# Kernel tuning notes

Measured on AMD Instinct MI355X. Metric: run time of the kernel, lower is better.

The kernel has to match this reference:

```python
import jax, jax.numpy as jnp
import numpy as np

N = 100000   # nodes
E = 400000   # edges
P = 250000   # permutations (substructures)
L = 16       # lrp_length
D = 16       # lrp_out_dim
M = P * L    # perm-length rows of the sparse gather matrices


def setup_inputs() -> dict:
    key = jax.random.key(0)
    ks = jax.random.split(key, 16)
    return {
        "nfeat": jax.random.normal(ks[0], (N, D), dtype=jnp.float32),
        "efeat_idx": jax.random.randint(ks[1], (E,), 0, 4, dtype=jnp.int64),
        "n_row": jnp.arange(M, dtype=jnp.int64),
        "n_col": jax.random.randint(ks[2], (M,), 0, N, dtype=jnp.int64),
        "n_val": jax.random.uniform(ks[3], (M,), dtype=jnp.float32),
        "e_row": jnp.arange(M, dtype=jnp.int64),
        "e_col": jax.random.randint(ks[4], (M,), 0, E, dtype=jnp.int64),
        "e_val": jax.random.uniform(ks[5], (M,), dtype=jnp.float32),
        "p_row": jax.random.randint(ks[6], (P,), 0, N, dtype=jnp.int64),
        "p_col": jnp.arange(P, dtype=jnp.int64),
        "p_val": jax.random.uniform(ks[7], (P,), dtype=jnp.float32),
        "degs": jax.random.uniform(ks[8], (N,), dtype=jnp.float32) * 10.0,
        "weights": jax.random.normal(ks[9], (D, D, L), dtype=jnp.float32),
        "bias": jnp.zeros((1, D), dtype=jnp.float32),
        "W0": jax.random.normal(ks[10], (1, 2 * D), dtype=jnp.float32),
        "b0": jnp.zeros((2 * D,), dtype=jnp.float32),
        "W1": jax.random.normal(ks[11], (2 * D, D), dtype=jnp.float32),
        "b1": jnp.zeros((D,), dtype=jnp.float32),
        "bond_emb": jax.random.normal(ks[12], (4, D), dtype=jnp.float32),
    }


def _spmm(row, col, val, mat, m):
    # torch_sparse.spmm(index, value, m, n, mat): out[r] += val * mat[c]
    return jax.ops.segment_sum(val[:, None] * mat[col], row, num_segments=m)


def reference(nfeat, efeat_idx, n_row, n_col, n_val, e_row, e_col, e_val,
              p_row, p_col, p_val, degs, weights, bias, W0, b0, W1, b1, bond_emb):
    efeat = bond_emb[efeat_idx]                              # [E, D]
    x = _spmm(n_row, n_col, n_val, nfeat, M) \
        + _spmm(e_row, e_col, e_val, efeat, M)               # [M, D], M = P*L
    # transpose(0,1).view(D, -1, L).permute(1, 2, 0) -> [P, L, D]
    x = x.T.reshape(D, P, L).transpose(1, 2, 0)
    # einsum('dab,bca->dc'): d=P, a=L, b=D_in, c=D_out
    x = jax.nn.relu(jnp.einsum('pld,dcl->pc', x, weights) + bias)  # [P, D]
    pooled = _spmm(p_row, p_col, p_val, x, N)                # [N, D]
    # degree gate MLP: 1 -> 2D -> D
    fd = jax.nn.relu(degs[:, None] @ W0 + b0) @ W1 + b1      # [N, D]
    return pooled * fd
```

## Files before the change

### kernel.cpp

```cpp
#include <hip/hip_runtime.h>

#define NP 250000
#define NN 100000
#define NE 400000
#define LL 16
#define DD 16
#define MM (NP * LL)
#define NTILES (NP / 16)
#define PERM_BLOCKS 512
#define GWAVES (PERM_BLOCKS * 4)

typedef __bf16 bf16x8 __attribute__((ext_vector_type(8)));
typedef float  f32x4  __attribute__((ext_vector_type(4)));
typedef int    i32x4  __attribute__((ext_vector_type(4)));

__device__ __forceinline__ float4 fma4(float a, float4 b, float4 c) {
    float4 r;
    r.x = fmaf(a, b.x, c.x);
    r.y = fmaf(a, b.y, c.y);
    r.z = fmaf(a, b.z, c.z);
    r.w = fmaf(a, b.w, c.w);
    return r;
}

__global__ __launch_bounds__(256) void init_kernel(
    const float* __restrict__ w,
    const float* __restrict__ nfeat,
    const float* __restrict__ bond_emb,
    const int* __restrict__ e_col,
    const int* __restrict__ efeat_idx,
    const float* __restrict__ degs,
    const float* __restrict__ W0,
    const float* __restrict__ b0,
    const float* __restrict__ W1,
    const float* __restrict__ b1,
    __bf16* __restrict__ wfrag,
    __bf16* __restrict__ nfeat_bf,
    __bf16* __restrict__ bond_bf,
    unsigned char* __restrict__ be2,
    float* __restrict__ fd,
    float* __restrict__ out)
{
    int t = blockIdx.x * 256 + threadIdx.x;
    if (t < 4096) {
        int kb = t >> 9;
        int lane = (t >> 3) & 63;
        int j = t & 7;
        int quad = lane >> 4, c = lane & 15;
        int d = ((quad & 1) << 3) + j;
        int l = ((quad >> 1) << 3) + kb;
        wfrag[t] = (__bf16)w[d * 256 + c * 16 + l];
    }
    if (t < NN * DD) {
        nfeat_bf[t] = (__bf16)nfeat[t];
        out[t] = 0.f;
    }
    if (t < 64) bond_bf[t] = (__bf16)bond_emb[t];
    if (t < MM / 4) {
        int4 ec = *(const int4*)(e_col + t * 4);
        unsigned int c0 = (unsigned int)efeat_idx[ec.x] & 3u;
        unsigned int c1 = (unsigned int)efeat_idx[ec.y] & 3u;
        unsigned int c2 = (unsigned int)efeat_idx[ec.z] & 3u;
        unsigned int c3 = (unsigned int)efeat_idx[ec.w] & 3u;
        be2[t] = (unsigned char)(c0 | (c1 << 2) | (c2 << 4) | (c3 << 6));
    }
    if (fd != nullptr && t < NN) {
        float dg = degs[t];
        float4 a0 = ((const float4*)b1)[0];
        float4 a1 = ((const float4*)b1)[1];
        float4 a2 = ((const float4*)b1)[2];
        float4 a3 = ((const float4*)b1)[3];
#pragma unroll
        for (int j2 = 0; j2 < 32; ++j2) {
            float h = fmaxf(fmaf(dg, W0[j2], b0[j2]), 0.f);
            const float4* w1r = (const float4*)(W1 + j2 * 16);
            a0 = fma4(h, w1r[0], a0);
            a1 = fma4(h, w1r[1], a1);
            a2 = fma4(h, w1r[2], a2);
            a3 = fma4(h, w1r[3], a3);
        }
        float4* o = (float4*)(fd + (size_t)t * DD);
        o[0] = a0; o[1] = a1; o[2] = a2; o[3] = a3;
    }
}


struct Early { i32x4 nca, ncb, pr; };
struct Late  { f32x4 nva, nvb, eva, evb, pv; unsigned int be16; };
struct Gath  { bf16x8 nfr[8]; float gv[4]; int prs[4]; };

__device__ __forceinline__ void load_early(Early& e, int tile, int col, int lhalf, int quad,
        const int* __restrict__ n_col, const int* __restrict__ p_row) {
    const int pbase = tile * 16;
    const int mbase = (pbase + col) * LL + lhalf * 8;
    e.nca = __builtin_nontemporal_load((const i32x4*)(n_col + mbase));
    e.ncb = __builtin_nontemporal_load((const i32x4*)(n_col + mbase + 4));
    e.pr  = __builtin_nontemporal_load((const i32x4*)(p_row + pbase + quad * 4));
}

__device__ __forceinline__ void load_late(Late& lt, int tile, int col, int lhalf, int quad,
        const float* __restrict__ n_val, const float* __restrict__ e_val,
        const unsigned char* __restrict__ be2, const float* __restrict__ p_val) {
    const int pbase = tile * 16;
    const int mbase = (pbase + col) * LL + lhalf * 8;
    lt.nva = __builtin_nontemporal_load((const f32x4*)(n_val + mbase));
    lt.nvb = __builtin_nontemporal_load((const f32x4*)(n_val + mbase + 4));
    lt.eva = __builtin_nontemporal_load((const f32x4*)(e_val + mbase));
    lt.evb = __builtin_nontemporal_load((const f32x4*)(e_val + mbase + 4));
    lt.pv  = __builtin_nontemporal_load((const f32x4*)(p_val + pbase + quad * 4));
    lt.be16 = (unsigned int)__builtin_nontemporal_load(
                  (const unsigned short*)(be2 + (mbase >> 2)));
}

__device__ __forceinline__ void issue_gathers(Gath& g, const Early& e,
        const __bf16* __restrict__ nfeat_bf, const float* __restrict__ fd,
        int half, int col) {
    int ncs[8] = {e.nca[0], e.nca[1], e.nca[2], e.nca[3],
                  e.ncb[0], e.ncb[1], e.ncb[2], e.ncb[3]};
#pragma unroll
    for (int kb = 0; kb < 8; ++kb)
        g.nfr[kb] = *(const bf16x8*)(nfeat_bf + (size_t)ncs[kb] * DD + half * 8);
#pragma unroll
    for (int r = 0; r < 4; ++r) {
        g.prs[r] = e.pr[r];
        g.gv[r] = fd ? fd[(size_t)e.pr[r] * DD + col] : 1.f;
    }
}

#define KSTEP(G, KB, NV, EV, J) do { \
    unsigned int b = (be >> (2 * (KB))) & 3u; \
    bf16x8 blo = (b & 1) ? bq1 : bq0; \
    bf16x8 bhi = (b & 1) ? bq3 : bq2; \
    bf16x8 bsel = (b & 2) ? bhi : blo; \
    float nv = (NV)[J], ev = (EV)[J]; \
    bf16x8 af; \
    _Pragma("unroll") \
    for (int j = 0; j < 8; ++j) \
        af[j] = (__bf16)fmaf(nv, (float)G.nfr[KB][j], ev * (float)bsel[j]); \
    acc = __builtin_amdgcn_mfma_f32_16x16x32_bf16(af, wf[KB], acc, 0, 0, 0); \
} while (0)

#define STEP(C, N) { \
    f32x4 acc = {0.f, 0.f, 0.f, 0.f}; \
    const unsigned int be = lat##C.be16; \
    KSTEP(g##C, 0, lat##C.nva, lat##C.eva, 0); \
    KSTEP(g##C, 1, lat##C.nva, lat##C.eva, 1); \
    KSTEP(g##C, 2, lat##C.nva, lat##C.eva, 2); \
    KSTEP(g##C, 3, lat##C.nva, lat##C.eva, 3); \
    if (tn < NTILES) issue_gathers(g##N, ear##N, nfeat_bf, fd, half, col); \
    if (tf < NTILES) load_early(ear##C, tf, col, lhalf, quad, n_col, p_row); \
    KSTEP(g##C, 4, lat##C.nvb, lat##C.evb, 0); \
    KSTEP(g##C, 5, lat##C.nvb, lat##C.evb, 1); \
    KSTEP(g##C, 6, lat##C.nvb, lat##C.evb, 2); \
    KSTEP(g##C, 7, lat##C.nvb, lat##C.evb, 3); \
    _Pragma("unroll") \
    for (int r = 0; r < 4; ++r) { \
        float v = fmaxf(acc[r] + bias_c, 0.f) * lat##C.pv[r] * g##C.gv[r]; \
        unsafeAtomicAdd(out + (size_t)g##C.prs[r] * DD + col, v); \
    } \
    if (tf < NTILES) load_late(lat##C, tf, col, lhalf, quad, n_val, e_val, be2, p_val); \
    if (tn >= NTILES) goto tail_done; \
    tn = tf; tf += GWAVES; \
}

__global__ __launch_bounds__(256) void perm_kernel(
    const __bf16* __restrict__ nfeat_bf,
    const int* __restrict__ n_col,
    const float* __restrict__ n_val,
    const float* __restrict__ e_val,
    const unsigned char* __restrict__ be2,
    const int* __restrict__ p_row,
    const float* __restrict__ p_val,
    const __bf16* __restrict__ wfrag,
    const float* __restrict__ bias,
    const __bf16* __restrict__ bond_bf,
    const float* __restrict__ fd,
    float* __restrict__ out)
{
    const int wid  = threadIdx.x >> 6;
    const int lane = threadIdx.x & 63;
    const int gw   = blockIdx.x * 4 + wid;
    const int quad = lane >> 4;
    const int col  = lane & 15;
    const int half = quad & 1;
    const int lhalf = quad >> 1;

    bf16x8 wf[8];
#pragma unroll
    for (int kb = 0; kb < 8; ++kb)
        wf[kb] = *(const bf16x8*)(wfrag + (kb * 64 + lane) * 8);
    const bf16x8 bq0 = *(const bf16x8*)(bond_bf + 0 * 16 + half * 8);
    const bf16x8 bq1 = *(const bf16x8*)(bond_bf + 1 * 16 + half * 8);
    const bf16x8 bq2 = *(const bf16x8*)(bond_bf + 2 * 16 + half * 8);
    const bf16x8 bq3 = *(const bf16x8*)(bond_bf + 3 * 16 + half * 8);
    const float bias_c = bias[col];

    Early earA, earB;
    Late  latA, latB;
    Gath  gA, gB;

    int tn = gw + GWAVES;
    int tf = tn + GWAVES;

    load_early(earA, gw, col, lhalf, quad, n_col, p_row);
    load_late (latA, gw, col, lhalf, quad, n_val, e_val, be2, p_val);
    if (tn < NTILES) load_early(earB, tn, col, lhalf, quad, n_col, p_row);
    issue_gathers(gA, earA, nfeat_bf, fd, half, col);
    if (tn < NTILES) load_late(latB, tn, col, lhalf, quad, n_val, e_val, be2, p_val);

    for (;;) {
        STEP(A, B);
        STEP(B, A);
    }
tail_done: ;
}

__global__ __launch_bounds__(256) void gate_kernel(
    const float* __restrict__ degs,
    const float* __restrict__ W0,
    const float* __restrict__ b0,
    const float* __restrict__ W1,
    const float* __restrict__ b1,
    float* __restrict__ out)
{
    int n = blockIdx.x * 256 + threadIdx.x;
    if (n >= NN) return;
    float dg = degs[n];
    float4 a0 = ((const float4*)b1)[0];
    float4 a1 = ((const float4*)b1)[1];
    float4 a2 = ((const float4*)b1)[2];
    float4 a3 = ((const float4*)b1)[3];
#pragma unroll
    for (int j = 0; j < 32; ++j) {
        float h = fmaxf(fmaf(dg, W0[j], b0[j]), 0.f);
        const float4* w1r = (const float4*)(W1 + j * 16);
        a0 = fma4(h, w1r[0], a0);
        a1 = fma4(h, w1r[1], a1);
        a2 = fma4(h, w1r[2], a2);
        a3 = fma4(h, w1r[3], a3);
    }
    float4* o = (float4*)(out + (size_t)n * DD);
    float4 v0 = o[0], v1 = o[1], v2 = o[2], v3 = o[3];
    v0.x *= a0.x; v0.y *= a0.y; v0.z *= a0.z; v0.w *= a0.w;
    v1.x *= a1.x; v1.y *= a1.y; v1.z *= a1.z; v1.w *= a1.w;
    v2.x *= a2.x; v2.y *= a2.y; v2.z *= a2.z; v2.w *= a2.w;
    v3.x *= a3.x; v3.y *= a3.y; v3.z *= a3.z; v3.w *= a3.w;
    o[0] = v0; o[1] = v1; o[2] = v2; o[3] = v3;
}

extern "C" void kernel_launch(void* const* d_in, const int* in_sizes, int n_in,
                              void* d_out, int out_size, void* d_ws, size_t ws_size,
                              hipStream_t stream) {
    const float* nfeat     = (const float*)d_in[0];
    const int*   efeat_idx = (const int*)d_in[1];
    const int*   n_col     = (const int*)d_in[3];
    const float* n_val     = (const float*)d_in[4];
    const int*   e_col     = (const int*)d_in[6];
    const float* e_val     = (const float*)d_in[7];
    const int*   p_row     = (const int*)d_in[8];
    const float* p_val     = (const float*)d_in[10];
    const float* degs      = (const float*)d_in[11];
    const float* weights   = (const float*)d_in[12];
    const float* bias      = (const float*)d_in[13];
    const float* W0        = (const float*)d_in[14];
    const float* b0        = (const float*)d_in[15];
    const float* W1        = (const float*)d_in[16];
    const float* b1        = (const float*)d_in[17];
    const float* bond_emb  = (const float*)d_in[18];

    float* out = (float*)d_out;

    char* wsb = (char*)d_ws;
    __bf16*        wfrag    = (__bf16*)wsb;
    __bf16*        nfeat_bf = (__bf16*)(wsb + 8192);
    __bf16*        bond_bf  = (__bf16*)(wsb + 8192 + 3200000);
    unsigned char* be2      = (unsigned char*)(wsb + 8192 + 3200000 + 128);
    const size_t base_need  = 8192 + 3200000 + 128 + 1000000;
    const bool   fuse_gate  = ws_size >= base_need + (size_t)NN * DD * 4;
    float*         fd       = fuse_gate ? (float*)(wsb + base_need) : nullptr;

    init_kernel<<<(NN * DD + 255) / 256, 256, 0, stream>>>(
        weights, nfeat, bond_emb, e_col, efeat_idx,
        degs, W0, b0, W1, b1,
        wfrag, nfeat_bf, bond_bf, be2, fd, out);

    perm_kernel<<<PERM_BLOCKS, 256, 0, stream>>>(
        nfeat_bf, n_col, n_val, e_val, be2, p_row, p_val,
        wfrag, bias, bond_bf, fd, out);

    if (!fuse_gate)
        gate_kernel<<<(NN + 255) / 256, 256, 0, stream>>>(degs, W0, b0, W1, b1, out);
}
```

Before: 204.5 us.

## Deepen software pipeline so gathers issue two tiles ahead of compute

```diff
diff --git a/kernel.cpp b/kernel.cpp
--- a/kernel.cpp
+++ b/kernel.cpp
@@ -86,8 +86,8 @@
 
 
 struct Early { i32x4 nca, ncb, pr; };
-struct Late  { f32x4 nva, nvb, eva, evb, pv; unsigned int be16; };
-struct Gath  { bf16x8 nfr[8]; float gv[4]; int prs[4]; };
+struct Gath  { bf16x8 nfr[8]; };
+struct Late  { f32x4 nva, nvb, eva, evb, pv, gv; i32x4 prs; unsigned int be16; };
 
 __device__ __forceinline__ void load_early(Early& e, int tile, int col, int lhalf, int quad,
         const int* __restrict__ n_col, const int* __restrict__ p_row) {
@@ -100,7 +100,8 @@
 
 __device__ __forceinline__ void load_late(Late& lt, int tile, int col, int lhalf, int quad,
         const float* __restrict__ n_val, const float* __restrict__ e_val,
-        const unsigned char* __restrict__ be2, const float* __restrict__ p_val) {
+        const unsigned char* __restrict__ be2, const float* __restrict__ p_val,
+        const Early& e, const float* __restrict__ fd) {
     const int pbase = tile * 16;
     const int mbase = (pbase + col) * LL + lhalf * 8;
     lt.nva = __builtin_nontemporal_load((const f32x4*)(n_val + mbase));
@@ -110,21 +111,19 @@
     lt.pv  = __builtin_nontemporal_load((const f32x4*)(p_val + pbase + quad * 4));
     lt.be16 = (unsigned int)__builtin_nontemporal_load(
                   (const unsigned short*)(be2 + (mbase >> 2)));
+    lt.prs = e.pr;
+#pragma unroll
+    for (int r = 0; r < 4; ++r)
+        lt.gv[r] = fd ? fd[(size_t)e.pr[r] * DD + col] : 1.f;
 }
 
 __device__ __forceinline__ void issue_gathers(Gath& g, const Early& e,
-        const __bf16* __restrict__ nfeat_bf, const float* __restrict__ fd,
-        int half, int col) {
+        const __bf16* __restrict__ nfeat_bf, int half) {
     int ncs[8] = {e.nca[0], e.nca[1], e.nca[2], e.nca[3],
                   e.ncb[0], e.ncb[1], e.ncb[2], e.ncb[3]};
 #pragma unroll
     for (int kb = 0; kb < 8; ++kb)
         g.nfr[kb] = *(const bf16x8*)(nfeat_bf + (size_t)ncs[kb] * DD + half * 8);
-#pragma unroll
-    for (int r = 0; r < 4; ++r) {
-        g.prs[r] = e.pr[r];
-        g.gv[r] = fd ? fd[(size_t)e.pr[r] * DD + col] : 1.f;
-    }
 }
 
 #define KSTEP(G, KB, NV, EV, J) do { \
@@ -147,20 +146,26 @@
     KSTEP(g##C, 1, lat##C.nva, lat##C.eva, 1); \
     KSTEP(g##C, 2, lat##C.nva, lat##C.eva, 2); \
     KSTEP(g##C, 3, lat##C.nva, lat##C.eva, 3); \
-    if (tn < NTILES) issue_gathers(g##N, ear##N, nfeat_bf, fd, half, col); \
-    if (tf < NTILES) load_early(ear##C, tf, col, lhalf, quad, n_col, p_row); \
+    { int te = tc + 3 * GWAVES; \
+      if (te < NTILES) load_early(ear##N, te, col, lhalf, quad, n_col, p_row); } \
     KSTEP(g##C, 4, lat##C.nvb, lat##C.evb, 0); \
     KSTEP(g##C, 5, lat##C.nvb, lat##C.evb, 1); \
     KSTEP(g##C, 6, lat##C.nvb, lat##C.evb, 2); \
     KSTEP(g##C, 7, lat##C.nvb, lat##C.evb, 3); \
+    f32x4 pvl = lat##C.pv, gvl = lat##C.gv; \
+    i32x4 prl = lat##C.prs; \
+    { int tg = tc + 2 * GWAVES; \
+      if (tg < NTILES) { \
+          issue_gathers(g##C, ear##C, nfeat_bf, half); \
+          load_late(lat##C, tg, col, lhalf, quad, n_val, e_val, be2, p_val, ear##C, fd); \
+      } } \
     _Pragma("unroll") \
     for (int r = 0; r < 4; ++r) { \
-        float v = fmaxf(acc[r] + bias_c, 0.f) * lat##C.pv[r] * g##C.gv[r]; \
-        unsafeAtomicAdd(out + (size_t)g##C.prs[r] * DD + col, v); \
+        float v = fmaxf(acc[r] + bias_c, 0.f) * pvl[r] * gvl[r]; \
+        unsafeAtomicAdd(out + (size_t)prl[r] * DD + col, v); \
     } \
-    if (tf < NTILES) load_late(lat##C, tf, col, lhalf, quad, n_val, e_val, be2, p_val); \
-    if (tn >= NTILES) goto tail_done; \
-    tn = tf; tf += GWAVES; \
+    tc += GWAVES; \
+    if (tc >= NTILES) goto tail_done; \
 }
 
 __global__ __launch_bounds__(256) void perm_kernel(
@@ -196,17 +201,18 @@
     const float bias_c = bias[col];
 
     Early earA, earB;
+    Gath  gA, gB;
     Late  latA, latB;
-    Gath  gA, gB;
-
-    int tn = gw + GWAVES;
-    int tf = tn + GWAVES;
-
-    load_early(earA, gw, col, lhalf, quad, n_col, p_row);
-    load_late (latA, gw, col, lhalf, quad, n_val, e_val, be2, p_val);
-    if (tn < NTILES) load_early(earB, tn, col, lhalf, quad, n_col, p_row);
-    issue_gathers(gA, earA, nfeat_bf, fd, half, col);
-    if (tn < NTILES) load_late(latB, tn, col, lhalf, quad, n_val, e_val, be2, p_val);
+
+    int tc = gw;
+
+    load_early(earA, tc, col, lhalf, quad, n_col, p_row);
+    load_early(earB, tc + GWAVES, col, lhalf, quad, n_col, p_row);
+    issue_gathers(gA, earA, nfeat_bf, half);
+    load_late(latA, tc, col, lhalf, quad, n_val, e_val, be2, p_val, earA, fd);
+    load_early(earA, tc + 2 * GWAVES, col, lhalf, quad, n_col, p_row);
+    issue_gathers(gB, earB, nfeat_bf, half);
+    load_late(latB, tc + GWAVES, col, lhalf, quad, n_val, e_val, be2, p_val, earB, fd);
 
     for (;;) {
         STEP(A, B);
```

New measurement: 205.6 us. Within noise of the previous version (+0.6%).
